# Kernel tuning notes

Measured on AMD Instinct MI355X. Metric: run time of the kernel, lower is better.

## Reference

```python
import jax, jax.numpy as jnp
import numpy as np
from jax import lax


def _gelu(x):
    return jax.nn.gelu(x, approximate=False)  # torch nn.GELU default = exact erf


def _ln_cf(x, g, b, eps=1e-6):
    # channels_first LayerNorm over dim 1 (biased variance, as in the source)
    m = x.mean(1, keepdims=True)
    v = ((x - m) ** 2).mean(1, keepdims=True)
    return g[None, :, None, None] * ((x - m) / jnp.sqrt(v + eps)) + b[None, :, None, None]


def _conv1x1(x, w):
    return jnp.einsum('bihw,oi->bohw', x, w[:, :, 0, 0])


def _conv3x3(x, w, d):
    # 3x3 conv, padding=dilation=d, no bias
    return lax.conv_general_dilated(x, w, (1, 1), [(d, d), (d, d)], rhs_dilation=(d, d),
                                    dimension_numbers=('NCHW', 'OIHW', 'NCHW'))


def _forward(x, conv1_w, conv1_b, conv2_w, conv2_b,
             cw_w1, cw_b1, cw_ln_g, cw_ln_b, cw_w2, cw_b2,
             aspp0_w, aspp0_g, aspp0_b, aspp1_w, aspp1_g, aspp1_b,
             aspp2_w, aspp2_g, aspp2_b, aspp3_w, aspp3_g, aspp3_b,
             asppp_w, asppp_g, asppp_b, proj_w, proj_g, proj_b):
    B, C, H, W = x.shape
    # x1 = conv1(x)
    x1 = _conv1x1(x, conv1_w) + conv1_b[None, :, None, None]
    # ChannelWeighting
    avg = x.mean((2, 3))                                    # [B,C]
    mx = x.max((2, 3))
    o = jnp.abs(avg - mx) * avg
    h = o @ cw_w1.T + cw_b1                                 # [B,Cout]
    mu = h.mean(-1, keepdims=True)
    vv = ((h - mu) ** 2).mean(-1, keepdims=True)
    h = cw_ln_g * ((h - mu) / jnp.sqrt(vv + 1e-5)) + cw_ln_b  # nn.LayerNorm eps=1e-5
    s = jax.nn.sigmoid(h @ cw_w2.T + cw_b2)                 # [B,C]
    xc = x * s[:, :, None, None] + x
    # ASPP (dropout in project is identity at eval)
    b0 = _gelu(_ln_cf(_conv1x1(xc, aspp0_w), aspp0_g, aspp0_b))
    b1 = _gelu(_ln_cf(_conv3x3(xc, aspp1_w, 3), aspp1_g, aspp1_b))
    b2 = _gelu(_ln_cf(_conv3x3(xc, aspp2_w, 6), aspp2_g, aspp2_b))
    b3 = _gelu(_ln_cf(_conv3x3(xc, aspp3_w, 9), aspp3_g, aspp3_b))
    gp = xc.mean((2, 3), keepdims=True)                     # AdaptiveAvgPool2d(1)
    bp = _gelu(_ln_cf(_conv1x1(gp, asppp_w), asppp_g, asppp_b))
    bp = jnp.broadcast_to(bp, (B, C, H, W))                 # bilinear 1x1->HxW == broadcast
    cat = jnp.concatenate([b0, b1, b2, b3, bp], axis=1)     # [B,5C,H,W]
    proj = _gelu(_ln_cf(_conv1x1(cat, proj_w), proj_g, proj_b))
    xa = _conv1x1(proj, conv1_w) + conv1_b[None, :, None, None]
    # AttentionModule, batched (redundant discarded Q@attn from source omitted)
    Co = xa.shape[1]
    HW = H * W
    P = x1.reshape(B, Co, HW)
    Q = xa.reshape(B, Co, HW)
    S = jnp.einsum('bcq,bcp->bqp', Q, P) / jnp.sqrt(jnp.asarray(HW, jnp.float32))
    A = jax.nn.softmax(S, axis=-1)                          # softmax over dim=1 of S[q,p] -> p
    L = jnp.einsum('bck,bkj->bcj', P, A).reshape(B, Co, H, W)
    O = L + xa
    return _conv1x1(O, conv2_w) + conv2_b[None, :, None, None]


def setup_inputs() -> dict:
    key = jax.random.key(0)
    ks = jax.random.split(key, 16)
    Cin, Cout, B, H, W = 256, 128, 4, 64, 64

    def nrm(k, shape, fan):
        return jax.random.normal(k, shape, jnp.float32) / np.float32(np.sqrt(fan))

    return {
        'x': jax.random.normal(ks[0], (B, Cin, H, W), jnp.float32),
        'conv1_w': nrm(ks[1], (Cout, Cin, 1, 1), Cin),
        'conv1_b': jnp.zeros((Cout,), jnp.float32),
        'conv2_w': nrm(ks[2], (Cin, Cout, 1, 1), Cout),
        'conv2_b': jnp.zeros((Cin,), jnp.float32),
        'cw_w1': nrm(ks[3], (Cout, Cin), Cin),
        'cw_b1': jnp.zeros((Cout,), jnp.float32),
        'cw_ln_g': jnp.ones((Cout,), jnp.float32),
        'cw_ln_b': jnp.zeros((Cout,), jnp.float32),
        'cw_w2': nrm(ks[4], (Cin, Cout), Cout),
        'cw_b2': jnp.zeros((Cin,), jnp.float32),
        'aspp0_w': nrm(ks[5], (Cin, Cin, 1, 1), Cin),
        'aspp0_g': jnp.ones((Cin,), jnp.float32),
        'aspp0_b': jnp.zeros((Cin,), jnp.float32),
        'aspp1_w': nrm(ks[6], (Cin, Cin, 3, 3), Cin * 9),
        'aspp1_g': jnp.ones((Cin,), jnp.float32),
        'aspp1_b': jnp.zeros((Cin,), jnp.float32),
        'aspp2_w': nrm(ks[7], (Cin, Cin, 3, 3), Cin * 9),
        'aspp2_g': jnp.ones((Cin,), jnp.float32),
        'aspp2_b': jnp.zeros((Cin,), jnp.float32),
        'aspp3_w': nrm(ks[8], (Cin, Cin, 3, 3), Cin * 9),
        'aspp3_g': jnp.ones((Cin,), jnp.float32),
        'aspp3_b': jnp.zeros((Cin,), jnp.float32),
        'asppp_w': nrm(ks[9], (Cin, Cin, 1, 1), Cin),
        'asppp_g': jnp.ones((Cin,), jnp.float32),
        'asppp_b': jnp.zeros((Cin,), jnp.float32),
        'proj_w': nrm(ks[10], (Cin, 5 * Cin, 1, 1), 5 * Cin),
        'proj_g': jnp.ones((Cin,), jnp.float32),
        'proj_b': jnp.zeros((Cin,), jnp.float32),
    }


def reference(x, conv1_w, conv1_b, conv2_w, conv2_b,
              cw_w1, cw_b1, cw_ln_g, cw_ln_b, cw_w2, cw_b2,
              aspp0_w, aspp0_g, aspp0_b, aspp1_w, aspp1_g, aspp1_b,
              aspp2_w, aspp2_g, aspp2_b, aspp3_w, aspp3_g, aspp3_b,
              asppp_w, asppp_g, asppp_b, proj_w, proj_g, proj_b):
    return _forward(x, conv1_w, conv1_b, conv2_w, conv2_b,
                    cw_w1, cw_b1, cw_ln_g, cw_ln_b, cw_w2, cw_b2,
                    aspp0_w, aspp0_g, aspp0_b, aspp1_w, aspp1_g, aspp1_b,
                    aspp2_w, aspp2_g, aspp2_b, aspp3_w, aspp3_g, aspp3_b,
                    asppp_w, asppp_g, asppp_b, proj_w, proj_g, proj_b)
```

## Files before the change

### kernel.cpp

```cpp
#include <hip/hip_runtime.h>
#include <hip/hip_bf16.h>
#include <math.h>

#define NB 4
#define CI 256
#define CO 128
#define HW 4096

typedef __attribute__((ext_vector_type(8))) short s8v;
typedef __attribute__((ext_vector_type(4))) short s4v;
typedef __attribute__((ext_vector_type(4))) float f4v;

__device__ __forceinline__ unsigned short f2bf(float f){
    __hip_bfloat16 h = __float2bfloat16(f);
    return *reinterpret_cast<unsigned short*>(&h);
}

__device__ __forceinline__ void lds_dma16(const void* g, void* l){
    __builtin_amdgcn_global_load_lds((const __attribute__((address_space(1))) unsigned int*)g,
                                     (__attribute__((address_space(3))) unsigned int*)l,
                                     16, 0, 0);
}

__device__ __forceinline__ float gelu_f(float x){
    float z  = x * 0.70710678118654752f;
    float az = fabsf(z);
    float tt = 1.f / (1.f + 0.3275911f * az);
    float poly = tt*(0.254829592f + tt*(-0.284496736f + tt*(1.421413741f +
                 tt*(-1.453152027f + tt*1.061405429f))));
    float erfv = 1.f - poly * __expf(-az*az);
    erfv = (z < 0.f) ? -erfv : erfv;
    return 0.5f * x * (1.f + erfv);
}

__global__ void k_pre(const float* __restrict__ x, float* __restrict__ avg, float* __restrict__ mx,
                      const float* __restrict__ c1, const float* __restrict__ a0,
                      const float* __restrict__ pj, const float* __restrict__ c2,
                      const float* __restrict__ d3, const float* __restrict__ d6,
                      const float* __restrict__ d9,
                      unsigned short* __restrict__ w_c1, unsigned short* __restrict__ w_a0,
                      unsigned short* __restrict__ w_pj, unsigned short* __restrict__ w_c2,
                      unsigned short* __restrict__ w_d3, unsigned short* __restrict__ w_d6,
                      unsigned short* __restrict__ w_d9){
    int blk = blockIdx.x;
    int t = threadIdx.x;
    if (blk < 1024){
        const float* p = x + (long long)blk * HW;
        float s = 0.f, m = -1e30f;
        for (int i = t; i < HW; i += 256){ float v = p[i]; s += v; m = fmaxf(m, v); }
        __shared__ float ss[256], sm[256];
        ss[t] = s; sm[t] = m; __syncthreads();
        for (int o = 128; o > 0; o >>= 1){
            if (t < o){ ss[t] += ss[t+o]; sm[t] = fmaxf(sm[t], sm[t+o]); }
            __syncthreads();
        }
        if (t == 0){ avg[blk] = ss[0] / (float)HW; mx[blk] = sm[0]; }
        return;
    }
    int i = (blk - 1024)*256 + t;
    if (i < 458752){
        if (i < 32768)        w_c1[i]        = f2bf(c1[i]);
        else if (i < 98304)   w_a0[i-32768]  = f2bf(a0[i-32768]);
        else if (i < 425984)  w_pj[i-98304]  = f2bf(pj[i-98304]);
        else                  w_c2[i-425984] = f2bf(c2[i-425984]);
    } else {
        int j = i - 458752;
        int which = j / 589824;
        int l = j - which*589824;
        int tap = l >> 16, rem = l & 65535, o = rem >> 8, ci = rem & 255;
        const float* src = (which==0) ? d3 : ((which==1) ? d6 : d9);
        unsigned short* dst = (which==0) ? w_d3 : ((which==1) ? w_d6 : w_d9);
        dst[l] = f2bf(src[o*2304 + ci*9 + tap]);
    }
}

__global__ void k_cw(const float* __restrict__ avg, const float* __restrict__ mx,
                     const float* __restrict__ w1, const float* __restrict__ b1,
                     const float* __restrict__ lng, const float* __restrict__ lnb,
                     const float* __restrict__ w2, const float* __restrict__ b2,
                     float* __restrict__ sv, float* __restrict__ gp,
                     float* __restrict__ zb){
    int b = blockIdx.x, t = threadIdx.x;
    if (b == 0) zb[t] = 0.f;
    __shared__ float o_s[256];
    __shared__ float h_s[128];
    __shared__ float stat[2];
    float a = avg[b*256 + t];
    o_s[t] = fabsf(a - mx[b*256 + t]) * a;
    __syncthreads();
    if (t < 128){
        float h = b1[t];
        for (int i = 0; i < 256; i++) h += o_s[i] * w1[t*256 + i];
        h_s[t] = h;
    }
    __syncthreads();
    if (t == 0){
        float s = 0.f, s2 = 0.f;
        for (int j = 0; j < 128; j++){ s += h_s[j]; s2 += h_s[j]*h_s[j]; }
        float mean = s / 128.f;
        float var  = s2 / 128.f - mean*mean;
        stat[0] = mean; stat[1] = rsqrtf(var + 1e-5f);
    }
    __syncthreads();
    if (t < 128) h_s[t] = lng[t] * ((h_s[t] - stat[0]) * stat[1]) + lnb[t];
    __syncthreads();
    float z = b2[t];
    for (int j = 0; j < 128; j++) z += h_s[j] * w2[t*128 + j];
    float sig = 1.f / (1.f + __expf(-z));
    sv[b*256 + t] = sig;
    gp[b*256 + t] = a * (1.f + sig);
}

__global__ void k_xT(const float* __restrict__ x, const float* __restrict__ sv,
                     unsigned short* __restrict__ xT, unsigned short* __restrict__ xcT){
    int b = blockIdx.z, c0 = blockIdx.y*64, h0 = blockIdx.x*64;
    __shared__ unsigned short T1[64][66], T2[64][66];
    int t = threadIdx.x;
    int hl = t & 63, cs = t >> 6;
    #pragma unroll
    for (int r = 0; r < 16; r++){
        int c = cs*16 + r;
        float v = x[((long long)b*256 + c0 + c)*HW + h0 + hl];
        float sc = 1.f + sv[b*256 + c0 + c];
        T1[c][hl] = f2bf(v);
        T2[c][hl] = f2bf(v*sc);
    }
    __syncthreads();
    int cl = t & 63, hs = t >> 6;
    #pragma unroll
    for (int r = 0; r < 16; r++){
        int h = hs*16 + r;
        long long o = ((long long)b*HW + h0 + h)*256 + c0 + cl;
        xT[o]  = T1[cl][h];
        xcT[o] = T2[cl][h];
    }
}

__device__ __forceinline__ void ln_epi32(f4v acc[2][2],
        int b, int n0, int w, int lane, int m, int q, int t,
        const float* Gs, const float* Bts,
        float (*Psum)[32], float (*Psq)[32], float* Mn, float* Iv,
        unsigned short* __restrict__ outT, int outPitch, int colOff){
    float ls[2], ls2[2];
    #pragma unroll
    for (int ct = 0; ct < 2; ct++){
        float s = 0.f, s2 = 0.f;
        #pragma unroll
        for (int ms = 0; ms < 2; ms++)
            #pragma unroll
            for (int r = 0; r < 4; r++){ float v = acc[ms][ct][r]; s += v; s2 += v*v; }
        ls[ct] = s; ls2[ct] = s2;
    }
    #pragma unroll
    for (int ct = 0; ct < 2; ct++){
        ls[ct]  += __shfl_xor(ls[ct], 16);  ls[ct]  += __shfl_xor(ls[ct], 32);
        ls2[ct] += __shfl_xor(ls2[ct], 16); ls2[ct] += __shfl_xor(ls2[ct], 32);
    }
    if (lane < 16){
        #pragma unroll
        for (int ct = 0; ct < 2; ct++){ Psum[w][ct*16+lane] = ls[ct]; Psq[w][ct*16+lane] = ls2[ct]; }
    }
    __syncthreads();
    if (t < 32){
        float s = 0.f, s2 = 0.f;
        #pragma unroll
        for (int ww = 0; ww < 8; ww++){ s += Psum[ww][t]; s2 += Psq[ww][t]; }
        float mean = s * (1.f/256.f);
        Mn[t] = mean;
        Iv[t] = rsqrtf(s2*(1.f/256.f) - mean*mean + 1e-6f);
    }
    __syncthreads();
    #pragma unroll
    for (int ct = 0; ct < 2; ct++){
        int p = ct*16 + m;
        float mean = Mn[p], inv = Iv[p];
        long long rowb = ((long long)b*HW + n0 + p)*outPitch + colOff;
        #pragma unroll
        for (int ms = 0; ms < 2; ms++){
            s4v o4;
            #pragma unroll
            for (int r = 0; r < 4; r++){
                int c = w*32 + ms*16 + q*4 + r;
                float h = Gs[c]*((acc[ms][ct][r] - mean)*inv) + Bts[c];
                o4[r] = (short)f2bf(gelu_f(h));
            }
            *(s4v*)(outT + rowb + w*32 + ms*16 + q*4) = o4;
        }
    }
}

__global__ __launch_bounds__(512, 4)
void k_aspp(const unsigned short* __restrict__ w_a0, const unsigned short* __restrict__ w_d3,
            const unsigned short* __restrict__ w_d6, const unsigned short* __restrict__ w_d9,
            const unsigned short* __restrict__ BT,
            const float* __restrict__ a0_g, const float* __restrict__ a0_b,
            const float* __restrict__ a1_g, const float* __restrict__ a1_b,
            const float* __restrict__ a2_g, const float* __restrict__ a2_b,
            const float* __restrict__ a3_g, const float* __restrict__ a3_b,
            const float* __restrict__ gp, const float* __restrict__ ap_w,
            const float* __restrict__ ap_g, const float* __restrict__ ap_b,
            const float* __restrict__ zbuf,
            unsigned short* __restrict__ catT){
    int br = blockIdx.y, b = blockIdx.z;
    int t = threadIdx.x;
    __shared__ __align__(16) unsigned short As[256*64];
    __shared__ __align__(16) unsigned short Bs[128*64];
    __shared__ float Gs[256], Bts[256];
    if (br == 4){
        int p0 = blockIdx.x*128;
        float* z_s = (float*)As;
        unsigned short* bp_s = As + 2048;
        float* stat = (float*)(As + 4096);
        if (t < 256){
            float z = 0.f;
            for (int c = 0; c < 256; c++) z += gp[b*256 + c] * ap_w[t*256 + c];
            z_s[t] = z;
        }
        __syncthreads();
        if (t == 0){
            float s = 0.f, s2 = 0.f;
            for (int c = 0; c < 256; c++){ s += z_s[c]; s2 += z_s[c]*z_s[c]; }
            float mean = s / 256.f, var = s2 / 256.f - mean*mean;
            stat[0] = mean; stat[1] = rsqrtf(var + 1e-6f);
        }
        __syncthreads();
        if (t < 256){
            float h = ap_g[t] * ((z_s[t] - stat[0]) * stat[1]) + ap_b[t];
            bp_s[t] = f2bf(gelu_f(h));
        }
        __syncthreads();
        for (int it = 0; it < 8; it++){
            int i = it*512 + t;
            int pl = i >> 5, cj = (i & 31) * 8;
            s8v v8;
            #pragma unroll
            for (int k2 = 0; k2 < 8; k2++) v8[k2] = (short)bp_s[cj + k2];
            *(s8v*)(catT + ((long long)b*HW + p0 + pl)*1280 + 1024 + cj) = v8;
        }
        return;
    }
    int n0 = blockIdx.x * 128;
    const unsigned short* BTb = BT + (long long)b*HW*256;
    const unsigned short* A  = (br==0) ? w_a0 : (br==1) ? w_d3 : (br==2) ? w_d6 : w_d9;
    const float* g   = (br==0) ? a0_g : (br==1) ? a1_g : (br==2) ? a2_g : a3_g;
    const float* bta = (br==0) ? a0_b : (br==1) ? a1_b : (br==2) ? a2_b : a3_b;
    int d    = (br==0) ? 0 : (br==1) ? 3 : (br==2) ? 6 : 9;
    int NS   = (br==0) ? 4 : 36;
    if (t < 256){ Gs[t] = g[t]; Bts[t] = bta[t]; }

    int w = t>>6, lane = t&63, m = lane&15, q = lane>>4;
    int wr = w>>1, wc = w&1;
    int rsw = m&7;
    int rl8 = lane>>3;
    int gch = (lane&7) ^ rl8;
    int aoff = rl8*256 + gch*8;
    int y0 = n0 >> 6;

    f4v acc[4][4];
    #pragma unroll
    for (int ms = 0; ms < 4; ms++)
        #pragma unroll
        for (int ct = 0; ct < 4; ct++){ f4v z = {0.f,0.f,0.f,0.f}; acc[ms][ct] = z; }

    for (int s = 0; s < NS; ++s){
        int tap = s>>2, kc = s&3;
        int dy = tap/3 - 1, dx = tap%3 - 1;
        const unsigned short* abase = A + tap*65536 + kc*64 + aoff;
        #pragma unroll
        for (int i = 0; i < 4; i++){
            int row0 = w*32 + i*8;
            lds_dma16(abase + row0*256, &As[row0*64]);
        }
        int xadd = rl8 + dx*d;
        #pragma unroll
        for (int i = 0; i < 2; i++){
            int bn0 = w*16 + i*8;
            int yy = y0 + (bn0>>6) + dy*d;
            int xs = (bn0 & 63) + xadd;
            const unsigned short* gsrc = ((unsigned)yy < 64u && (unsigned)xs < 64u)
                ? (BTb + (long long)(yy*64 + xs)*256 + kc*64 + gch*8)
                : (const unsigned short*)zbuf;
            lds_dma16(gsrc, &Bs[bn0*64]);
        }
        __syncthreads();
        #pragma unroll
        for (int ks = 0; ks < 2; ks++){
            s8v bfr[4];
            #pragma unroll
            for (int ct = 0; ct < 4; ct++)
                bfr[ct] = *(const s8v*)&Bs[(wc*64 + ct*16 + m)*64 + ((q + 4*ks) ^ rsw)*8];
            #pragma unroll
            for (int ms = 0; ms < 4; ms++){
                s8v afr = *(const s8v*)&As[(wr*64 + ms*16 + m)*64 + ((q + 4*ks) ^ rsw)*8];
                #pragma unroll
                for (int ct = 0; ct < 4; ct++)
                    acc[ms][ct] = __builtin_amdgcn_mfma_f32_16x16x32_bf16(afr, bfr[ct], acc[ms][ct], 0,0,0);
            }
        }
        __syncthreads();
    }
    float* Psum = (float*)Bs;
    float* Psq  = Psum + 512;
    float* Mn   = Psq  + 512;
    float* Iv   = Mn   + 128;
    #pragma unroll
    for (int ct = 0; ct < 4; ct++){
        float s = 0.f, s2 = 0.f;
        #pragma unroll
        for (int ms = 0; ms < 4; ms++)
            #pragma unroll
            for (int r = 0; r < 4; r++){ float v = acc[ms][ct][r]; s += v; s2 += v*v; }
        s  += __shfl_xor(s, 16);  s  += __shfl_xor(s, 32);
        s2 += __shfl_xor(s2, 16); s2 += __shfl_xor(s2, 32);
        if (lane < 16){
            Psum[wr*128 + wc*64 + ct*16 + lane] = s;
            Psq [wr*128 + wc*64 + ct*16 + lane] = s2;
        }
    }
    __syncthreads();
    if (t < 128){
        float s  = Psum[t] + Psum[128+t] + Psum[256+t] + Psum[384+t];
        float s2 = Psq [t] + Psq [128+t] + Psq [256+t] + Psq [384+t];
        float mean = s * (1.f/256.f);
        Mn[t] = mean;
        Iv[t] = rsqrtf(s2*(1.f/256.f) - mean*mean + 1e-6f);
    }
    __syncthreads();
    #pragma unroll
    for (int ct = 0; ct < 4; ct++){
        int p = wc*64 + ct*16 + m;
        float mean = Mn[p], inv = Iv[p];
        long long rowb = ((long long)b*HW + n0 + p)*1280 + br*256;
        #pragma unroll
        for (int ms = 0; ms < 4; ms++){
            s4v o4;
            #pragma unroll
            for (int r = 0; r < 4; r++){
                int c = wr*64 + ms*16 + q*4 + r;
                float h = Gs[c]*((acc[ms][ct][r] - mean)*inv) + Bts[c];
                o4[r] = (short)f2bf(gelu_f(h));
            }
            *(s4v*)(catT + rowb + wr*64 + ms*16 + q*4) = o4;
        }
    }
}

__global__ __launch_bounds__(512)
void k_branch1(const unsigned short* __restrict__ A, int K,
               const unsigned short* __restrict__ BT,
               const float* __restrict__ g, const float* __restrict__ beta,
               unsigned short* __restrict__ outT, int outPitch, int colOff){
    int b = blockIdx.y, n0 = blockIdx.x*32;
    const unsigned short* BTb = BT + (long long)b*HW*K;
    __shared__ __align__(16) unsigned short As[2][256*64];
    __shared__ __align__(16) unsigned short Bs[2][32*64];
    __shared__ float Psum[8][32], Psq[8][32], Mn[32], Iv[32];
    __shared__ float Gs[256], Bts[256];
    int t = threadIdx.x, w = t>>6, lane = t&63, m = lane&15, q = lane>>4;
    int rl8 = lane>>3, gch = (lane&7) ^ rl8, rsw = m&7;
    if (t < 256){ Gs[t] = g[t]; Bts[t] = beta[t]; }
    f4v acc[2][2];
    #pragma unroll
    for (int ms = 0; ms < 2; ms++)
        #pragma unroll
        for (int ct = 0; ct < 2; ct++){ f4v z = {0.f,0.f,0.f,0.f}; acc[ms][ct] = z; }
    const int NSt = K >> 6;
    auto issue = [&](int s, int buf){
        int k0 = s*64;
        #pragma unroll
        for (int i = 0; i < 4; i++){
            int ar = w*32 + i*8;
            lds_dma16(A + (long long)(ar + rl8)*K + k0 + gch*8, &As[buf][ar*64]);
        }
        if (w < 4)
            lds_dma16(BTb + (long long)(n0 + w*8 + rl8)*K + k0 + gch*8, &Bs[buf][w*8*64]);
    };
    issue(0, 0);
    for (int s = 0; s < NSt; ++s){
        int cur = s & 1;
        if (s+1 < NSt){
            issue(s+1, cur^1);
            if (w < 4) asm volatile("s_waitcnt vmcnt(5)" ::: "memory");
            else       asm volatile("s_waitcnt vmcnt(4)" ::: "memory");
        } else {
            asm volatile("s_waitcnt vmcnt(0)" ::: "memory");
        }
        __builtin_amdgcn_s_barrier();
        __builtin_amdgcn_sched_barrier(0);
        const unsigned short* Ac = &As[cur][0];
        const unsigned short* Bc = &Bs[cur][0];
        #pragma unroll
        for (int ks = 0; ks < 2; ks++){
            s8v bfr[2];
            #pragma unroll
            for (int ct = 0; ct < 2; ct++)
                bfr[ct] = *(const s8v*)&Bc[(ct*16 + m)*64 + ((q + 4*ks) ^ rsw)*8];
            #pragma unroll
            for (int ms = 0; ms < 2; ms++){
                s8v afr = *(const s8v*)&Ac[(w*32 + ms*16 + m)*64 + ((q + 4*ks) ^ rsw)*8];
                #pragma unroll
                for (int ct = 0; ct < 2; ct++)
                    acc[ms][ct] = __builtin_amdgcn_mfma_f32_16x16x32_bf16(afr, bfr[ct], acc[ms][ct], 0,0,0);
            }
        }
        __builtin_amdgcn_s_barrier();
        __builtin_amdgcn_sched_barrier(0);
    }
    __syncthreads();
    ln_epi32(acc, b, n0, w, lane, m, q, t, Gs, Bts, Psum, Psq, Mn, Iv, outT, outPitch, colOff);
}

__global__ __launch_bounds__(256)
void k_conv1m(const unsigned short* __restrict__ A,
              const unsigned short* __restrict__ BT,
              const float* __restrict__ bias,
              unsigned short* __restrict__ outT,
              unsigned short* __restrict__ outC,
              float* __restrict__ outF){
    int b = blockIdx.y, n0 = blockIdx.x*32;
    const unsigned short* BTb = BT + (long long)b*HW*256;
    __shared__ __align__(16) unsigned short As[128*64];
    __shared__ __align__(16) unsigned short Bs[32*64];
    int t = threadIdx.x, w = t>>6, lane = t&63, m = lane&15, q = lane>>4;
    int rl8 = lane>>3, gch = (lane&7) ^ rl8, rsw = m&7;
    f4v acc[2][2];
    #pragma unroll
    for (int ms = 0; ms < 2; ms++)
        #pragma unroll
        for (int ct = 0; ct < 2; ct++){ f4v z = {0.f,0.f,0.f,0.f}; acc[ms][ct] = z; }
    for (int k0 = 0; k0 < 256; k0 += 64){
        #pragma unroll
        for (int i = 0; i < 4; i++){
            int ar = w*32 + i*8;
            lds_dma16(A + (long long)(ar + rl8)*256 + k0 + gch*8, &As[ar*64]);
        }
        lds_dma16(BTb + (long long)(n0 + w*8 + rl8)*256 + k0 + gch*8, &Bs[w*8*64]);
        __syncthreads();
        #pragma unroll
        for (int ks = 0; ks < 2; ks++){
            s8v bfr[2];
            #pragma unroll
            for (int ct = 0; ct < 2; ct++)
                bfr[ct] = *(const s8v*)&Bs[(ct*16 + m)*64 + ((q + 4*ks) ^ rsw)*8];
            #pragma unroll
            for (int ms = 0; ms < 2; ms++){
                s8v afr = *(const s8v*)&As[(w*32 + ms*16 + m)*64 + ((q + 4*ks) ^ rsw)*8];
                #pragma unroll
                for (int ct = 0; ct < 2; ct++)
                    acc[ms][ct] = __builtin_amdgcn_mfma_f32_16x16x32_bf16(afr, bfr[ct], acc[ms][ct], 0,0,0);
            }
        }
        __syncthreads();
    }
    #pragma unroll
    for (int ct = 0; ct < 2; ct++){
        int p = n0 + ct*16 + m;
        #pragma unroll
        for (int ms = 0; ms < 2; ms++){
            s4v o4;
            float vals[4];
            #pragma unroll
            for (int r = 0; r < 4; r++){
                int c = w*32 + ms*16 + q*4 + r;
                vals[r] = acc[ms][ct][r] + bias[c];
                o4[r] = (short)f2bf(vals[r]);
            }
            *(s4v*)(outT + ((long long)b*HW + p)*128 + w*32 + ms*16 + q*4) = o4;
            if (outC){
                #pragma unroll
                for (int r = 0; r < 4; r++){
                    int c = w*32 + ms*16 + q*4 + r;
                    outC[((long long)b*128 + c)*HW + p] = (unsigned short)o4[r];
                }
            }
            if (outF){
                #pragma unroll
                for (int r = 0; r < 4; r++){
                    int c = w*32 + ms*16 + q*4 + r;
                    outF[((long long)b*128 + c)*HW + p] = vals[r];
                }
            }
        }
    }
}

__global__ __launch_bounds__(256)
void k_attn_stats3(const unsigned short* __restrict__ QT,
                   const unsigned short* __restrict__ PT,
                   float* __restrict__ lpart){
    int b = blockIdx.z, jc = blockIdx.y, k0 = blockIdx.x * 128;
    const unsigned short* QTb = QT + (long long)b * HW * CO;
    const unsigned short* PTb = PT + (long long)b * HW * CO;
    __shared__ unsigned short Ps[2][64][132];
    int t = threadIdx.x;
    int w = t >> 6, lane = t & 63, m = lane & 15, q = lane >> 4;
    s8v a[2][4];
    #pragma unroll
    for (int kh = 0; kh < 2; kh++)
        #pragma unroll
        for (int ks = 0; ks < 4; ks++)
            a[kh][ks] = *(const s8v*)(QTb + (long long)(k0 + kh*64 + w*16 + m) * CO + q*8 + ks*32);
    float rl[2][4];
    #pragma unroll
    for (int kh = 0; kh < 2; kh++)
        #pragma unroll
        for (int r = 0; r < 4; r++) rl[kh][r] = 0.f;
    const float scale = 0.015625f;
    int jbase = jc * 1024;
    int sr = t >> 2, sch = t & 3;
    uint4 pf[4];
    {   const uint4* src = (const uint4*)(PTb + (long long)(jbase + sr) * CO + sch * 32);
        #pragma unroll
        for (int i = 0; i < 4; i++) pf[i] = src[i];
    }
    for (int jt = 0; jt < 16; jt++){
        int cur = jt & 1;
        {   uint4* dst = (uint4*)&Ps[cur][sr][sch * 32];
            #pragma unroll
            for (int i = 0; i < 4; i++) dst[i] = pf[i];
        }
        __syncthreads();
        if (jt < 15){
            const uint4* src = (const uint4*)(PTb + (long long)(jbase + (jt+1)*64 + sr) * CO + sch * 32);
            #pragma unroll
            for (int i = 0; i < 4; i++) pf[i] = src[i];
        }
        #pragma unroll
        for (int kh = 0; kh < 2; kh++){
            float sv[4][4];
            #pragma unroll
            for (int ct = 0; ct < 4; ct++){
                f4v acc = {0.f,0.f,0.f,0.f};
                #pragma unroll
                for (int ks = 0; ks < 4; ks++){
                    s8v bv = *(const s8v*)&Ps[cur][ct*16 + m][q*8 + ks*32];
                    acc = __builtin_amdgcn_mfma_f32_16x16x32_bf16(a[kh][ks], bv, acc, 0, 0, 0);
                }
                #pragma unroll
                for (int r = 0; r < 4; r++) sv[ct][r] = acc[r] * scale;
            }
            #pragma unroll
            for (int r = 0; r < 4; r++){
                float se = __expf(sv[0][r]) + __expf(sv[1][r])
                         + __expf(sv[2][r]) + __expf(sv[3][r]);
                #pragma unroll
                for (int msk = 1; msk < 16; msk <<= 1) se += __shfl_xor(se, msk);
                rl[kh][r] += se;
            }
        }
    }
    if (m == 0){
        #pragma unroll
        for (int kh = 0; kh < 2; kh++)
            #pragma unroll
            for (int r = 0; r < 4; r++){
                int k = k0 + kh*64 + w*16 + q*4 + r;
                lpart[(long long)jc * (NB*HW) + (long long)b*HW + k] = rl[kh][r];
            }
    }
}

__global__ __launch_bounds__(256)
void k_attn_apply2(const unsigned short* __restrict__ QT,
                   const unsigned short* __restrict__ PT,
                   const unsigned short* __restrict__ Pb,
                   const float* __restrict__ lpart,
                   float* __restrict__ Lp){
    int b = blockIdx.z, kc = blockIdx.y, j0 = blockIdx.x * 64;
    const unsigned short* QTb = QT + (long long)b * HW * CO;
    const unsigned short* PTb = PT + (long long)b * HW * CO;
    const unsigned short* Pbb = Pb + (long long)b * CO * HW;
    __shared__ __align__(16) unsigned short Qks[64*128];
    __shared__ __align__(16) unsigned short Pcs[128*64];
    __shared__ unsigned short Et[64][72];
    __shared__ float Il[2048];
    int t = threadIdx.x;
    int w = t >> 6, lane = t & 63, m = lane & 15, q = lane >> 4;
    int kbase = kc * 2048;
    int rl4 = lane >> 4;
    int rl8 = lane >> 3;
    int gch8 = (lane & 7) ^ rl8;
    {
        #pragma unroll
        for (int r = 0; r < 8; r++){
            int kl = t*8 + r;
            long long gi = (long long)b*HW + kbase + kl;
            float l = lpart[gi] + lpart[gi+16384] + lpart[gi+32768] + lpart[gi+49152];
            Il[kl] = 1.f / l;
        }
    }
    {
        #pragma unroll
        for (int i = 0; i < 4; i++){
            int rowb = w*16 + i*4;
            int gch = (lane & 15) ^ ((rowb & 15) + rl4);
            lds_dma16(PTb + (long long)(j0 + rowb + rl4)*CO + gch*8, &Qks[rowb*128]);
        }
        #pragma unroll
        for (int i = 0; i < 4; i++){
            int rowb = w*32 + i*8;
            lds_dma16(Pbb + (long long)(rowb + rl8)*HW + kbase + gch8*8, &Pcs[rowb*64]);
        }
    }
    asm volatile("s_waitcnt vmcnt(4) lgkmcnt(0)" ::: "memory");
    __builtin_amdgcn_s_barrier();
    __builtin_amdgcn_sched_barrier(0);
    s8v bj[4][4];
    #pragma unroll
    for (int ct = 0; ct < 4; ct++)
        #pragma unroll
        for (int ks = 0; ks < 4; ks++)
            bj[ct][ks] = *(const s8v*)&Qks[(ct*16 + m)*128 + ((q + 4*ks) ^ m)*8];
    asm volatile("s_waitcnt lgkmcnt(0)" ::: "memory");
    __builtin_amdgcn_s_barrier();
    __builtin_amdgcn_sched_barrier(0);
    {
        #pragma unroll
        for (int i = 0; i < 4; i++){
            int rowb = w*16 + i*4;
            int gch = (lane & 15) ^ ((rowb & 15) + rl4);
            lds_dma16(QTb + (long long)(kbase + rowb + rl4)*CO + gch*8, &Qks[rowb*128]);
        }
    }
    f4v accL[2][4];
    #pragma unroll
    for (int mt = 0; mt < 2; mt++)
        #pragma unroll
        for (int ct = 0; ct < 4; ct++){ f4v z = {0.f,0.f,0.f,0.f}; accL[mt][ct] = z; }
    const float scale = 0.015625f;
    for (int kt = 0; kt < 32; kt++){
        int k0 = kbase + kt*64;
        if (kt == 0) asm volatile("s_waitcnt vmcnt(0)" ::: "memory");
        else         asm volatile("s_waitcnt vmcnt(4)" ::: "memory");
        __builtin_amdgcn_sched_barrier(0);
        s8v aS[4];
        #pragma unroll
        for (int ks = 0; ks < 4; ks++)
            aS[ks] = *(const s8v*)&Qks[(w*16 + m)*128 + ((q + 4*ks) ^ m)*8];
        float il[4];
        #pragma unroll
        for (int r = 0; r < 4; r++) il[r] = Il[kt*64 + w*16 + q*4 + r];
        #pragma unroll
        for (int ct = 0; ct < 4; ct++){
            f4v s = {0.f,0.f,0.f,0.f};
            #pragma unroll
            for (int ks = 0; ks < 4; ks++)
                s = __builtin_amdgcn_mfma_f32_16x16x32_bf16(aS[ks], bj[ct][ks], s, 0, 0, 0);
            s4v e4;
            #pragma unroll
            for (int r = 0; r < 4; r++)
                e4[r] = (short)f2bf(__expf(s[r]*scale) * il[r]);
            *(s4v*)&Et[ct*16 + m][w*16 + q*4] = e4;
        }
        if (kt+1 < 32){
            #pragma unroll
            for (int i = 0; i < 4; i++){
                int rowb = w*16 + i*4;
                int gch = (lane & 15) ^ ((rowb & 15) + rl4);
                lds_dma16(QTb + (long long)(k0 + 64 + rowb + rl4)*CO + gch*8, &Qks[rowb*128]);
            }
        }
        asm volatile("s_waitcnt lgkmcnt(0)" ::: "memory");
        __builtin_amdgcn_s_barrier();
        __builtin_amdgcn_sched_barrier(0);
        asm volatile("s_waitcnt vmcnt(4)" ::: "memory");
        __builtin_amdgcn_sched_barrier(0);
        s8v aP[2][2];
        #pragma unroll
        for (int mt = 0; mt < 2; mt++)
            #pragma unroll
            for (int ks2 = 0; ks2 < 2; ks2++)
                aP[mt][ks2] = *(const s8v*)&Pcs[(w*32 + mt*16 + m)*64 + ((q + 4*ks2) ^ (m&7))*8];
        #pragma unroll
        for (int ct = 0; ct < 4; ct++){
            s8v bE0 = *(const s8v*)&Et[ct*16 + m][q*8];
            s8v bE1 = *(const s8v*)&Et[ct*16 + m][q*8 + 32];
            #pragma unroll
            for (int mt = 0; mt < 2; mt++){
                accL[mt][ct] = __builtin_amdgcn_mfma_f32_16x16x32_bf16(aP[mt][0], bE0, accL[mt][ct], 0, 0, 0);
                accL[mt][ct] = __builtin_amdgcn_mfma_f32_16x16x32_bf16(aP[mt][1], bE1, accL[mt][ct], 0, 0, 0);
            }
        }
        if (kt+1 < 32){
            #pragma unroll
            for (int i = 0; i < 4; i++){
                int rowb = w*32 + i*8;
                lds_dma16(Pbb + (long long)(rowb + rl8)*HW + k0 + 64 + gch8*8, &Pcs[rowb*64]);
            }
        }
        __builtin_amdgcn_s_barrier();
        __builtin_amdgcn_sched_barrier(0);
    }
    float* Lpb = Lp + ((long long)(kc*NB + b) * CO) * HW;
    #pragma unroll
    for (int mt = 0; mt < 2; mt++)
        #pragma unroll
        for (int ct = 0; ct < 4; ct++)
            #pragma unroll
            for (int r = 0; r < 4; r++){
                int c = w*32 + mt*16 + q*4 + r;
                Lpb[(long long)c*HW + j0 + ct*16 + m] = accL[mt][ct][r];
            }
}

__global__ __launch_bounds__(256)
void k_outfused(const unsigned short* __restrict__ A,
                const float* __restrict__ Lp, const float* __restrict__ xa,
                const float* __restrict__ bias, float* __restrict__ out){
    int b = blockIdx.y, j0 = blockIdx.x*32;
    __shared__ unsigned short Bs[32][136];
    __shared__ __align__(16) char pool[256*68*2];
    int t = threadIdx.x;
    {
        float* Bsf = (float*)pool;
        int c = t>>1, jh = t&1;
        long long base = ((long long)b*CO + c)*HW + j0 + jh*16;
        const long long csz = (long long)NB*CO*HW;
        float v[16];
        #pragma unroll
        for (int r = 0; r < 16; r++) v[r] = xa[base + r];
        #pragma unroll
        for (int pidx = 0; pidx < 2; pidx++){
            const float* src = Lp + pidx*csz + base;
            #pragma unroll
            for (int r = 0; r < 16; r++) v[r] += src[r];
        }
        #pragma unroll
        for (int r = 0; r < 16; r++) Bsf[c*33 + jh*16 + r] = v[r];
    }
    __syncthreads();
    {
        const float* Bsf = (const float*)pool;
        int j = t>>3, cs = t&7;
        #pragma unroll
        for (int r = 0; r < 16; r++){
            int c = cs*16 + r;
            Bs[j][c] = f2bf(Bsf[c*33 + j]);
        }
    }
    __syncthreads();
    unsigned short* As = (unsigned short*)pool;
    int w = t>>6, lane = t&63, m = lane&15, q = lane>>4;
    int rl8 = lane>>3, gch = (lane&7) ^ rl8, rsw = m&7;
    f4v acc[4][2];
    #pragma unroll
    for (int ms = 0; ms < 4; ms++)
        #pragma unroll
        for (int ct = 0; ct < 2; ct++){ f4v z = {0.f,0.f,0.f,0.f}; acc[ms][ct] = z; }
    for (int k0 = 0; k0 < 128; k0 += 64){
        __syncthreads();
        #pragma unroll
        for (int i = 0; i < 8; i++){
            int ar = w*64 + i*8;
            lds_dma16(A + (long long)(ar + rl8)*128 + k0 + gch*8, &As[ar*64]);
        }
        __syncthreads();
        #pragma unroll
        for (int ks = 0; ks < 2; ks++){
            s8v bfr[2];
            #pragma unroll
            for (int ct = 0; ct < 2; ct++) bfr[ct] = *(const s8v*)&Bs[ct*16+m][k0 + ks*32 + q*8];
            #pragma unroll
            for (int ms = 0; ms < 4; ms++){
                s8v afr = *(const s8v*)&As[(w*64 + ms*16 + m)*64 + ((q + 4*ks) ^ rsw)*8];
                #pragma unroll
                for (int ct = 0; ct < 2; ct++)
                    acc[ms][ct] = __builtin_amdgcn_mfma_f32_16x16x32_bf16(afr, bfr[ct], acc[ms][ct], 0,0,0);
            }
        }
    }
    #pragma unroll
    for (int ct = 0; ct < 2; ct++){
        int p = j0 + ct*16 + m;
        #pragma unroll
        for (int ms = 0; ms < 4; ms++)
            #pragma unroll
            for (int r = 0; r < 4; r++){
                int c = w*64 + ms*16 + q*4 + r;
                out[((long long)b*256 + c)*HW + p] = acc[ms][ct][r] + bias[c];
            }
    }
}

extern "C" void kernel_launch(void* const* d_in, const int* in_sizes, int n_in,
                              void* d_out, int out_size, void* d_ws, size_t ws_size,
                              hipStream_t stream) {
    const float* x       = (const float*)d_in[0];
    const float* conv1_w = (const float*)d_in[1];
    const float* conv1_b = (const float*)d_in[2];
    const float* conv2_w = (const float*)d_in[3];
    const float* conv2_b = (const float*)d_in[4];
    const float* cw_w1   = (const float*)d_in[5];
    const float* cw_b1   = (const float*)d_in[6];
    const float* cw_g    = (const float*)d_in[7];
    const float* cw_bt   = (const float*)d_in[8];
    const float* cw_w2   = (const float*)d_in[9];
    const float* cw_b2   = (const float*)d_in[10];
    const float* a0_w    = (const float*)d_in[11];
    const float* a0_g    = (const float*)d_in[12];
    const float* a0_b    = (const float*)d_in[13];
    const float* a1_w    = (const float*)d_in[14];
    const float* a1_g    = (const float*)d_in[15];
    const float* a1_b    = (const float*)d_in[16];
    const float* a2_w    = (const float*)d_in[17];
    const float* a2_g    = (const float*)d_in[18];
    const float* a2_b    = (const float*)d_in[19];
    const float* a3_w    = (const float*)d_in[20];
    const float* a3_g    = (const float*)d_in[21];
    const float* a3_b    = (const float*)d_in[22];
    const float* ap_w    = (const float*)d_in[23];
    const float* ap_g    = (const float*)d_in[24];
    const float* ap_b    = (const float*)d_in[25];
    const float* pj_w    = (const float*)d_in[26];
    const float* pj_g    = (const float*)d_in[27];
    const float* pj_b    = (const float*)d_in[28];
    float* out = (float*)d_out;

    float* ws    = (float*)d_ws;
    float* avg   = ws;
    float* mx    = ws + 1024;
    float* sv    = ws + 2048;
    float* gp    = ws + 3072;
    float* zbuf  = ws + 4096;
    float* xa    = ws + 37888;
    float* lpart = xa + 2097152;
    unsigned short* sb = (unsigned short*)(ws + 4232192);
    unsigned short* xT    = sb;
    unsigned short* xcT   = sb + 4194304;
    unsigned short* catT  = sb + 8388608;
    unsigned short* projT = sb + 29360128;
    unsigned short* P_bf  = sb + 33554432;
    unsigned short* PT_bf = sb + 35651584;
    unsigned short* QT_bf = sb + 37748736;
    unsigned short* w_c1  = sb + 41943040;
    unsigned short* w_a0  = sb + 41975808;
    unsigned short* w_pj  = sb + 42041344;
    unsigned short* w_c2  = sb + 42369024;
    unsigned short* w_d3  = sb + 42401792;
    unsigned short* w_d6  = sb + 42991616;
    unsigned short* w_d9  = sb + 43581440;
    float* Lp = (float*)catT;

    k_pre<<<dim3(9728), 256, 0, stream>>>(x, avg, mx,
                                          conv1_w, a0_w, pj_w, conv2_w, a1_w, a2_w, a3_w,
                                          w_c1, w_a0, w_pj, w_c2, w_d3, w_d6, w_d9);
    k_cw<<<dim3(NB), 256, 0, stream>>>(avg, mx, cw_w1, cw_b1, cw_g, cw_bt, cw_w2, cw_b2, sv, gp, zbuf);

    k_xT<<<dim3(64, 4, NB), 256, 0, stream>>>(x, sv, xT, xcT);

    k_conv1m<<<dim3(128, NB), 256, 0, stream>>>(w_c1, xT, conv1_b, PT_bf, P_bf, nullptr);

    k_aspp<<<dim3(32, 5, NB), 512, 0, stream>>>(w_a0, w_d3, w_d6, w_d9, xcT,
                                                a0_g, a0_b, a1_g, a1_b, a2_g, a2_b, a3_g, a3_b,
                                                gp, ap_w, ap_g, ap_b, zbuf, catT);

    k_branch1<<<dim3(128, NB), 512, 0, stream>>>(w_pj, 1280, catT, pj_g, pj_b, projT, 256, 0);

    k_conv1m<<<dim3(128, NB), 256, 0, stream>>>(w_c1, projT, conv1_b, QT_bf, nullptr, xa);

    k_attn_stats3<<<dim3(32, 4, NB), 256, 0, stream>>>(QT_bf, PT_bf, lpart);
    k_attn_apply2<<<dim3(64, 2, NB), 256, 0, stream>>>(QT_bf, PT_bf, P_bf, lpart, Lp);

    k_outfused<<<dim3(128, NB), 256, 0, stream>>>(w_c2, Lp, xa, conv2_b, out);

    (void)in_sizes; (void)n_in; (void)out_size; (void)ws_size;
}
```

Baseline: 375.1 us.

## Double-buffer ASPP LDS loads and schedule heavy dilated branches first

The ASPP GEMM loop now uses two LDS stages. The next step's weight and activation DMA is issued before computing on the current one, with explicit vmcnt waits and raw barriers replacing the two __syncthreads per step. Blocks are also reordered so the three 36-step dilated branches take the low blockIdx.y values and the 4-step 1x1 branch runs last, with a slot map keeping the output columns correct. Doubling LDS per block means fewer resident blocks, so the launch bound occupancy hint drops from 4 to 2.

```diff
diff --git a/kernel.cpp b/kernel.cpp
--- a/kernel.cpp
+++ b/kernel.cpp
@@ -189,7 +189,7 @@
     }
 }
 
-__global__ __launch_bounds__(512, 4)
+__global__ __launch_bounds__(512, 2)
 void k_aspp(const unsigned short* __restrict__ w_a0, const unsigned short* __restrict__ w_d3,
             const unsigned short* __restrict__ w_d6, const unsigned short* __restrict__ w_d9,
             const unsigned short* __restrict__ BT,
@@ -203,14 +203,13 @@
             unsigned short* __restrict__ catT){
     int br = blockIdx.y, b = blockIdx.z;
     int t = threadIdx.x;
-    __shared__ __align__(16) unsigned short As[256*64];
-    __shared__ __align__(16) unsigned short Bs[128*64];
+    __shared__ __align__(16) unsigned short SB[2][24576];
     __shared__ float Gs[256], Bts[256];
     if (br == 4){
         int p0 = blockIdx.x*128;
-        float* z_s = (float*)As;
-        unsigned short* bp_s = As + 2048;
-        float* stat = (float*)(As + 4096);
+        float* z_s = (float*)&SB[0][0];
+        unsigned short* bp_s = &SB[0][2048];
+        float* stat = (float*)&SB[0][4096];
         if (t < 256){
             float z = 0.f;
             for (int c = 0; c < 256; c++) z += gp[b*256 + c] * ap_w[t*256 + c];
@@ -241,11 +240,12 @@
     }
     int n0 = blockIdx.x * 128;
     const unsigned short* BTb = BT + (long long)b*HW*256;
-    const unsigned short* A  = (br==0) ? w_a0 : (br==1) ? w_d3 : (br==2) ? w_d6 : w_d9;
-    const float* g   = (br==0) ? a0_g : (br==1) ? a1_g : (br==2) ? a2_g : a3_g;
-    const float* bta = (br==0) ? a0_b : (br==1) ? a1_b : (br==2) ? a2_b : a3_b;
-    int d    = (br==0) ? 0 : (br==1) ? 3 : (br==2) ? 6 : 9;
-    int NS   = (br==0) ? 4 : 36;
+    const unsigned short* A  = (br==0) ? w_d3 : (br==1) ? w_d6 : (br==2) ? w_d9 : w_a0;
+    const float* g   = (br==0) ? a1_g : (br==1) ? a2_g : (br==2) ? a3_g : a0_g;
+    const float* bta = (br==0) ? a1_b : (br==1) ? a2_b : (br==2) ? a3_b : a0_b;
+    int d    = (br==0) ? 3 : (br==1) ? 6 : (br==2) ? 9 : 0;
+    int slot = (br==3) ? 0 : (br+1);
+    int NS   = (br==3) ? 4 : 36;
     if (t < 256){ Gs[t] = g[t]; Bts[t] = bta[t]; }
 
     int w = t>>6, lane = t&63, m = lane&15, q = lane>>4;
@@ -262,14 +262,15 @@
         #pragma unroll
         for (int ct = 0; ct < 4; ct++){ f4v z = {0.f,0.f,0.f,0.f}; acc[ms][ct] = z; }
 
-    for (int s = 0; s < NS; ++s){
+    auto issue = [&](int s, int buf){
         int tap = s>>2, kc = s&3;
-        int dy = tap/3 - 1, dx = tap%3 - 1;
+        int dy = tap/3 - 1, dx = tap - (tap/3)*3 - 1;
+        unsigned short* dst = &SB[buf][0];
         const unsigned short* abase = A + tap*65536 + kc*64 + aoff;
         #pragma unroll
         for (int i = 0; i < 4; i++){
             int row0 = w*32 + i*8;
-            lds_dma16(abase + row0*256, &As[row0*64]);
+            lds_dma16(abase + row0*256, dst + row0*64);
         }
         int xadd = rl8 + dx*d;
         #pragma unroll
@@ -280,26 +281,41 @@
             const unsigned short* gsrc = ((unsigned)yy < 64u && (unsigned)xs < 64u)
                 ? (BTb + (long long)(yy*64 + xs)*256 + kc*64 + gch*8)
                 : (const unsigned short*)zbuf;
-            lds_dma16(gsrc, &Bs[bn0*64]);
-        }
-        __syncthreads();
+            lds_dma16(gsrc, dst + 16384 + bn0*64);
+        }
+    };
+
+    issue(0, 0);
+    for (int s = 0; s < NS; ++s){
+        int cur = s & 1;
+        if (s+1 < NS){
+            issue(s+1, cur^1);
+            asm volatile("s_waitcnt vmcnt(6)" ::: "memory");
+        } else {
+            asm volatile("s_waitcnt vmcnt(0)" ::: "memory");
+        }
+        __builtin_amdgcn_s_barrier();
+        __builtin_amdgcn_sched_barrier(0);
+        const unsigned short* Ac = &SB[cur][0];
+        const unsigned short* Bc = &SB[cur][16384];
         #pragma unroll
         for (int ks = 0; ks < 2; ks++){
             s8v bfr[4];
             #pragma unroll
             for (int ct = 0; ct < 4; ct++)
-                bfr[ct] = *(const s8v*)&Bs[(wc*64 + ct*16 + m)*64 + ((q + 4*ks) ^ rsw)*8];
+                bfr[ct] = *(const s8v*)&Bc[(wc*64 + ct*16 + m)*64 + ((q + 4*ks) ^ rsw)*8];
             #pragma unroll
             for (int ms = 0; ms < 4; ms++){
-                s8v afr = *(const s8v*)&As[(wr*64 + ms*16 + m)*64 + ((q + 4*ks) ^ rsw)*8];
+                s8v afr = *(const s8v*)&Ac[(wr*64 + ms*16 + m)*64 + ((q + 4*ks) ^ rsw)*8];
                 #pragma unroll
                 for (int ct = 0; ct < 4; ct++)
                     acc[ms][ct] = __builtin_amdgcn_mfma_f32_16x16x32_bf16(afr, bfr[ct], acc[ms][ct], 0,0,0);
             }
         }
-        __syncthreads();
-    }
-    float* Psum = (float*)Bs;
+        __builtin_amdgcn_s_barrier();
+        __builtin_amdgcn_sched_barrier(0);
+    }
+    float* Psum = (float*)&SB[0][0];
     float* Psq  = Psum + 512;
     float* Mn   = Psq  + 512;
     float* Iv   = Mn   + 128;
@@ -330,7 +346,7 @@
     for (int ct = 0; ct < 4; ct++){
         int p = wc*64 + ct*16 + m;
         float mean = Mn[p], inv = Iv[p];
-        long long rowb = ((long long)b*HW + n0 + p)*1280 + br*256;
+        long long rowb = ((long long)b*HW + n0 + p)*1280 + slot*256;
         #pragma unroll
         for (int ms = 0; ms < 4; ms++){
             s4v o4;
```

New measurement: 396.2 us. +5.6%, slower.
